# Kernel tuning notes

Hardware: AMD Instinct MI355X
Metric: run time of the kernel (lower is better)

Reference implementation:

```python
import jax, jax.numpy as jnp
import numpy as np

B, T, H, S = 64, 512, 768, 128  # batch, seq_len, hidden_size, num_statements


def setup_inputs() -> dict:
    key = jax.random.key(0)
    ks = jax.random.split(key, 6)
    hidden = jax.random.normal(ks[0], (B, T, H), dtype=jnp.float32)
    # per-token statement ids, sorted (statements appear contiguously in source order)
    statements_ids = jnp.sort(jax.random.randint(ks[1], (B, T), 0, S), axis=-1).astype(jnp.int32)
    scale = 1.0 / np.sqrt(H)
    w1 = jax.random.normal(ks[2], (H, H), dtype=jnp.float32) * scale
    b1 = jnp.zeros((H,), dtype=jnp.float32)
    w2 = jax.random.normal(ks[3], (H, H), dtype=jnp.float32) * scale
    b2 = jnp.zeros((H,), dtype=jnp.float32)
    w3 = jax.random.normal(ks[4], (H, 1), dtype=jnp.float32) * scale
    b3 = jnp.zeros((1,), dtype=jnp.float32)
    return {"hidden": hidden, "statements_ids": statements_ids,
            "w1": w1, "b1": b1, "w2": w2, "b2": b2, "w3": w3, "b3": b3}


def _segment_mean(x, sid):
    # x: [T, H], sid: [T] -> [S, H] mean of tokens per statement id
    sums = jax.ops.segment_sum(x, sid, num_segments=S)            # [S, H]
    cnts = jax.ops.segment_sum(jnp.ones((x.shape[0],), x.dtype), sid, num_segments=S)  # [S]
    return sums / jnp.maximum(cnts, 1.0)[:, None]


def reference(hidden, statements_ids, w1, b1, w2, b2, w3, b3):
    # per-statement mean pooling (scatter-mean), vectorized over batch
    pooled = jax.vmap(_segment_mean)(hidden, statements_ids)      # [B, S, H]
    # CodeCoverageMLP: fc1 -> GELU -> fc2 -> GELU -> fc3 -> sigmoid (dropout = eval identity)
    x = jax.nn.gelu(pooled @ w1 + b1, approximate=False)
    x = jax.nn.gelu(x @ w2 + b2, approximate=False)
    preds = jax.nn.sigmoid(x @ w3 + b3)                           # [B, S, 1]
    return preds[..., 0]                                          # [B, S]
```

## Files before the change

kernel.cpp:

```cpp
#include <hip/hip_runtime.h>
#include <stdint.h>

#define NB 64
#define NT 512
#define NH 768
#define NS 128
#define NM (NB*NS)

typedef _Float16 half8 __attribute__((ext_vector_type(8)));
typedef _Float16 half4 __attribute__((ext_vector_type(4)));
typedef __attribute__((ext_vector_type(4))) float f32x4;

__device__ __forceinline__ float gelu_fast(float x) {
  float ax = fabsf(x) * 0.70710678118654752440f;
  float t  = __builtin_amdgcn_rcpf(1.0f + 0.3275911f * ax);
  float e  = __expf(-ax * ax);
  float poly = t * (0.254829592f + t * (-0.284496736f +
               t * (1.421413741f + t * (-1.453152027f + t * 1.061405429f))));
  float erfv = 1.0f - poly * e;
  float phi  = 0.5f * (1.0f + copysignf(erfv, x));
  return x * phi;
}

__device__ __forceinline__ void gll16(const void* g, void* l) {
  __builtin_amdgcn_global_load_lds(
      (__attribute__((address_space(1))) unsigned int*)g,
      (__attribute__((address_space(3))) unsigned int*)l,
      16, 0, 0);
}

__global__ void prep_w_kernel(const float* __restrict__ w1, const float* __restrict__ w2,
                              _Float16* __restrict__ W) {
  int id = blockIdx.x * 256 + threadIdx.x;
  int n  = id % NH;
  int t  = id / NH;
  int kc = t % 96;
  int w  = t / 96;
  const float* src = w ? w2 : w1;
  int k0 = kc * 8;
  half8 h;
#pragma unroll
  for (int i = 0; i < 8; ++i)
    h[i] = (_Float16)src[(size_t)(k0 + i) * NH + n];
  const size_t off = ((((size_t)w * 48 + (n >> 4)) * 96 + kc) * 16 + (n & 15)) * 8;
  *(half8*)&W[off] = h;
}

__global__ __launch_bounds__(192)
void pool_kernel(const float* __restrict__ hidden, const int* __restrict__ sid,
                 _Float16* __restrict__ Ahi, _Float16* __restrict__ Alo) {
  __shared__ int   s_sid[NT];
  __shared__ short s_e0[NS + 1];
  __shared__ float sAcc[8][NH];
  const int b = blockIdx.y, g = blockIdx.x;
  const int tid = threadIdx.x;

  for (int t = tid; t < NT; t += 192) s_sid[t] = sid[b * NT + t];
  __syncthreads();
  for (int t = tid; t < NT; t += 192) {
    const int cur  = s_sid[t];
    const int prev = t ? s_sid[t - 1] : -1;
    for (int s = prev + 1; s <= cur; ++s) s_e0[s] = (short)t;
    if (t == NT - 1)
      for (int s = cur + 1; s <= NS; ++s) s_e0[s] = (short)NT;
  }
#pragma unroll
  for (int i = 0; i < 8; ++i)
    *(f32x4*)&sAcc[0][(i * 192 + tid) * 4] = (f32x4){0.f, 0.f, 0.f, 0.f};
  __syncthreads();

  const int s0 = g * 8;
  const int t0 = s_e0[s0], t1 = s_e0[s0 + 8];
  const int col = tid * 4;
  const float* hb = hidden + (size_t)b * NT * NH + col;

  if (t1 > t0) {
    constexpr int D = 8;
    f32x4 buf[D];
#pragma unroll
    for (int j = 0; j < D; ++j) {
      int tj = t0 + j; if (tj >= t1) tj = t1 - 1;
      buf[j] = *(const f32x4*)(hb + (size_t)tj * NH);
    }
    f32x4 acc = {0.f, 0.f, 0.f, 0.f};
    int cur = s_sid[t0];
    int t = t0;
    for (; t + D <= t1; t += D) {
#pragma unroll
      for (int j = 0; j < D; ++j) {
        f32x4 v = buf[j];
        int tn = t + j + D; if (tn >= t1) tn = t1 - 1;
        buf[j] = *(const f32x4*)(hb + (size_t)tn * NH);
        const int s = s_sid[t + j];
        if (s != cur) {
          *(f32x4*)&sAcc[cur - s0][col] = acc;
          acc = (f32x4){0.f, 0.f, 0.f, 0.f};
          cur = s;
        }
        acc += v;
      }
    }
#pragma unroll
    for (int j = 0; j < D; ++j) {
      if (t + j < t1) {
        f32x4 v = buf[j];
        const int s = s_sid[t + j];
        if (s != cur) {
          *(f32x4*)&sAcc[cur - s0][col] = acc;
          acc = (f32x4){0.f, 0.f, 0.f, 0.f};
          cur = s;
        }
        acc += v;
      }
    }
    *(f32x4*)&sAcc[cur - s0][col] = acc;
  }
  __syncthreads();

#pragma unroll
  for (int s = 0; s < 8; ++s) {
    const int gs = s0 + s;
    const int cnt = s_e0[gs + 1] - s_e0[gs];
    const float inv = 1.0f / (float)(cnt > 0 ? cnt : 1);
    f32x4 v = *(const f32x4*)&sAcc[s][col];
    half4 h, l;
#pragma unroll
    for (int j = 0; j < 4; ++j) {
      float x = v[j] * inv;
      h[j] = (_Float16)x;
      l[j] = (_Float16)(x - (float)h[j]);
    }
    const size_t off = (size_t)(b * NS + gs) * NH + col;
    *(half4*)&Ahi[off] = h;
    *(half4*)&Alo[off] = l;
  }
}

__global__ __launch_bounds__(512, 4)
void mlp_kernel(const _Float16* __restrict__ Ahi, const _Float16* __restrict__ Alo,
                const _Float16* __restrict__ Wp,
                const float* __restrict__ b1, const float* __restrict__ b2,
                const float* __restrict__ w3, const float* __restrict__ b3,
                float* __restrict__ out) {
  __shared__ _Float16 sA[2][4096];
  __shared__ _Float16 sX[32 * NH];
  float (*sP)[32] = (float(*)[32])&sA[0][0];

  const int tid  = threadIdx.x;
  const int lane = tid & 63;
  const int wv   = tid >> 6;
  const int lr   = lane & 15;
  const int lk4  = lane >> 4;
  const int row0 = blockIdx.x * 32;

  const _Float16* W1 = Wp;
  const _Float16* W2 = Wp + (size_t)NH * NH;

  const int str  = wv * 4 + lk4;
  const int scol = (lr * 8) ^ ((str & 7) << 3);
#define STAGE(kt) {                                                           \
    const size_t src = (size_t)(row0 + str) * NH + (kt) * 128 + scol;         \
    gll16(Ahi + src, &sA[0][wv * 512]);                                       \
    gll16(Alo + src, &sA[1][wv * 512]); }

  f32x4 acc1[2][6] = {};
  STAGE(0);
  __syncthreads();
  for (int kt = 0; kt < 6; ++kt) {
    half8 bw[6], bwn[6];
#pragma unroll
    for (int nf = 0; nf < 6; ++nf)
      bw[nf] = *(const half8*)(W1 + ((size_t)(wv * 6 + nf) * 96 + kt * 16 + lk4) * 128 + lr * 8);
#pragma unroll
    for (int kk = 0; kk < 4; ++kk) {
      if (kk < 3) {
#pragma unroll
        for (int nf = 0; nf < 6; ++nf)
          bwn[nf] = *(const half8*)(W1 + ((size_t)(wv * 6 + nf) * 96 + kt * 16 + (kk + 1) * 4 + lk4) * 128 + lr * 8);
      }
#pragma unroll
      for (int mf = 0; mf < 2; ++mf) {
        const int ar = mf * 16 + lr;
        const int ad = ar * 128 + ((kk * 32 + lk4 * 8) ^ ((ar & 7) << 3));
        half8 ah = *(const half8*)&sA[0][ad];
        half8 al = *(const half8*)&sA[1][ad];
#pragma unroll
        for (int nf = 0; nf < 6; ++nf) {
          acc1[mf][nf] = __builtin_amdgcn_mfma_f32_16x16x32_f16(ah, bw[nf], acc1[mf][nf], 0, 0, 0);
          acc1[mf][nf] = __builtin_amdgcn_mfma_f32_16x16x32_f16(al, bw[nf], acc1[mf][nf], 0, 0, 0);
        }
      }
#pragma unroll
      for (int nf = 0; nf < 6; ++nf) bw[nf] = bwn[nf];
    }
    __syncthreads();
    if (kt < 5) {
      STAGE(kt + 1);
      __syncthreads();
    }
  }

#pragma unroll
  for (int nf = 0; nf < 6; ++nf) {
    const int col = wv * 96 + nf * 16 + lr;
    const float bv = b1[col];
#pragma unroll
    for (int mf = 0; mf < 2; ++mf)
#pragma unroll
      for (int r = 0; r < 4; ++r) {
        const int row = mf * 16 + lk4 * 4 + r;
        sX[row * NH + (col ^ ((row & 7) << 3))] = (_Float16)gelu_fast(acc1[mf][nf][r] + bv);
      }
  }
  __syncthreads();

  f32x4 acc2[2][6] = {};
  half8 bw2[6], bw2n[6];
#pragma unroll
  for (int nf = 0; nf < 6; ++nf)
    bw2[nf] = *(const half8*)(W2 + ((size_t)(wv * 6 + nf) * 96 + lk4) * 128 + lr * 8);
  for (int g = 0; g < 24; ++g) {
    if (g < 23) {
#pragma unroll
      for (int nf = 0; nf < 6; ++nf)
        bw2n[nf] = *(const half8*)(W2 + ((size_t)(wv * 6 + nf) * 96 + (g + 1) * 4 + lk4) * 128 + lr * 8);
    }
    const int koff = g * 32 + lk4 * 8;
#pragma unroll
    for (int mf = 0; mf < 2; ++mf) {
      const int ar = mf * 16 + lr;
      half8 a = *(const half8*)&sX[ar * NH + (koff ^ ((ar & 7) << 3))];
#pragma unroll
      for (int nf = 0; nf < 6; ++nf)
        acc2[mf][nf] = __builtin_amdgcn_mfma_f32_16x16x32_f16(a, bw2[nf], acc2[mf][nf], 0, 0, 0);
    }
#pragma unroll
    for (int nf = 0; nf < 6; ++nf) bw2[nf] = bw2n[nf];
  }

  float p[2][4] = {};
#pragma unroll
  for (int nf = 0; nf < 6; ++nf) {
    const int col = wv * 96 + nf * 16 + lr;
    const float bv = b2[col], wvv = w3[col];
#pragma unroll
    for (int mf = 0; mf < 2; ++mf)
#pragma unroll
      for (int r = 0; r < 4; ++r)
        p[mf][r] += gelu_fast(acc2[mf][nf][r] + bv) * wvv;
  }
#pragma unroll
  for (int mf = 0; mf < 2; ++mf)
#pragma unroll
    for (int r = 0; r < 4; ++r) {
      float v = p[mf][r];
      v += __shfl_xor(v, 1, 16);
      v += __shfl_xor(v, 2, 16);
      v += __shfl_xor(v, 4, 16);
      v += __shfl_xor(v, 8, 16);
      if (lr == 0) sP[wv][mf * 16 + lk4 * 4 + r] = v;
    }
  __syncthreads();
  if (tid < 32) {
    float s = b3[0];
#pragma unroll
    for (int w = 0; w < 8; ++w) s += sP[w][tid];
    out[row0 + tid] = 1.0f / (1.0f + expf(-s));
  }
#undef STAGE
}

extern "C" void kernel_launch(void* const* d_in, const int* in_sizes, int n_in,
                              void* d_out, int out_size, void* d_ws, size_t ws_size,
                              hipStream_t stream) {
  (void)in_sizes; (void)n_in; (void)out_size; (void)ws_size;
  const float* hidden = (const float*)d_in[0];
  const int*   sid    = (const int*)d_in[1];
  const float* w1     = (const float*)d_in[2];
  const float* b1     = (const float*)d_in[3];
  const float* w2     = (const float*)d_in[4];
  const float* b2     = (const float*)d_in[5];
  const float* w3     = (const float*)d_in[6];
  const float* b3     = (const float*)d_in[7];
  float* out = (float*)d_out;

  char* p = (char*)d_ws;
  const size_t actE = (size_t)NM * NH;
  _Float16* Ahi = (_Float16*)p; p += actE * 2;
  _Float16* Alo = (_Float16*)p; p += actE * 2;
  _Float16* W   = (_Float16*)p; p += (size_t)2 * NH * NH * 2;

  prep_w_kernel<<<2 * 96 * NH / 256, 256, 0, stream>>>(w1, w2, W);
  pool_kernel<<<dim3(16, NB), 192, 0, stream>>>(hidden, sid, Ahi, Alo);
  mlp_kernel<<<NM / 32, 512, 0, stream>>>(Ahi, Alo, W, b1, b2, w3, b3, out);
}
```

Baseline: 216.4 us.

## Fuse segment-mean pooling into MLP kernel, keeping pooled activations in LDS

```diff
diff --git a/kernel.cpp b/kernel.cpp
--- a/kernel.cpp
+++ b/kernel.cpp
@@ -20,13 +20,6 @@
   float erfv = 1.0f - poly * e;
   float phi  = 0.5f * (1.0f + copysignf(erfv, x));
   return x * phi;
-}
-
-__device__ __forceinline__ void gll16(const void* g, void* l) {
-  __builtin_amdgcn_global_load_lds(
-      (__attribute__((address_space(1))) unsigned int*)g,
-      (__attribute__((address_space(3))) unsigned int*)l,
-      16, 0, 0);
 }
 
 __global__ void prep_w_kernel(const float* __restrict__ w1, const float* __restrict__ w2,
@@ -46,18 +39,29 @@
   *(half8*)&W[off] = h;
 }
 
-__global__ __launch_bounds__(192)
-void pool_kernel(const float* __restrict__ hidden, const int* __restrict__ sid,
-                 _Float16* __restrict__ Ahi, _Float16* __restrict__ Alo) {
-  __shared__ int   s_sid[NT];
-  __shared__ short s_e0[NS + 1];
-  __shared__ float sAcc[8][NH];
-  const int b = blockIdx.y, g = blockIdx.x;
-  const int tid = threadIdx.x;
-
-  for (int t = tid; t < NT; t += 192) s_sid[t] = sid[b * NT + t];
-  __syncthreads();
-  for (int t = tid; t < NT; t += 192) {
+__global__ __launch_bounds__(512)
+void fused_kernel(const float* __restrict__ hidden, const int* __restrict__ sid,
+                  const _Float16* __restrict__ Wp,
+                  const float* __restrict__ b1, const float* __restrict__ b2,
+                  const float* __restrict__ w3, const float* __restrict__ b3,
+                  float* __restrict__ out) {
+  __shared__ float    sAcc[32 * NH];
+  __shared__ _Float16 sX[32 * NH];
+  __shared__ int      s_sid[NT];
+  __shared__ short    s_e0[NS + 1];
+
+  const int tid  = threadIdx.x;
+  const int lane = tid & 63;
+  const int wv   = tid >> 6;
+  const int lr   = lane & 15;
+  const int lk4  = lane >> 4;
+  const int b  = blockIdx.y;
+  const int s0 = blockIdx.x * 32;
+
+  s_sid[tid] = sid[b * NT + tid];
+  __syncthreads();
+  {
+    const int t = tid;
     const int cur  = s_sid[t];
     const int prev = t ? s_sid[t - 1] : -1;
     for (int s = prev + 1; s <= cur; ++s) s_e0[s] = (short)t;
@@ -65,125 +69,111 @@
       for (int s = cur + 1; s <= NS; ++s) s_e0[s] = (short)NT;
   }
 #pragma unroll
-  for (int i = 0; i < 8; ++i)
-    *(f32x4*)&sAcc[0][(i * 192 + tid) * 4] = (f32x4){0.f, 0.f, 0.f, 0.f};
-  __syncthreads();
-
-  const int s0 = g * 8;
-  const int t0 = s_e0[s0], t1 = s_e0[s0 + 8];
-  const int col = tid * 4;
-  const float* hb = hidden + (size_t)b * NT * NH + col;
-
-  if (t1 > t0) {
-    constexpr int D = 8;
-    f32x4 buf[D];
-#pragma unroll
-    for (int j = 0; j < D; ++j) {
-      int tj = t0 + j; if (tj >= t1) tj = t1 - 1;
-      buf[j] = *(const f32x4*)(hb + (size_t)tj * NH);
-    }
-    f32x4 acc = {0.f, 0.f, 0.f, 0.f};
-    int cur = s_sid[t0];
-    int t = t0;
-    for (; t + D <= t1; t += D) {
+  for (int i = 0; i < 12; ++i)
+    *(f32x4*)&sAcc[(i * 512 + tid) * 4] = (f32x4){0.f, 0.f, 0.f, 0.f};
+  __syncthreads();
+
+  if (tid < 384) {
+    const int tg   = (tid >= 192) ? 1 : 0;
+    const int col  = (tid - tg * 192) * 4;
+    const int sg0  = s0 + tg * 16;
+    const int t0 = s_e0[sg0], t1 = s_e0[sg0 + 16];
+    const float* hb = hidden + (size_t)b * NT * NH + col;
+    if (t1 > t0) {
+      constexpr int D = 8;
+      f32x4 buf[D];
 #pragma unroll
       for (int j = 0; j < D; ++j) {
-        f32x4 v = buf[j];
-        int tn = t + j + D; if (tn >= t1) tn = t1 - 1;
-        buf[j] = *(const f32x4*)(hb + (size_t)tn * NH);
-        const int s = s_sid[t + j];
-        if (s != cur) {
-          *(f32x4*)&sAcc[cur - s0][col] = acc;
-          acc = (f32x4){0.f, 0.f, 0.f, 0.f};
-          cur = s;
+        int tj = t0 + j; if (tj >= t1) tj = t1 - 1;
+        buf[j] = *(const f32x4*)(hb + (size_t)tj * NH);
+      }
+      f32x4 acc = {0.f, 0.f, 0.f, 0.f};
+      int cur = s_sid[t0];
+      int t = t0;
+      for (; t + D <= t1; t += D) {
+#pragma unroll
+        for (int j = 0; j < D; ++j) {
+          f32x4 v = buf[j];
+          int tn = t + j + D; if (tn >= t1) tn = t1 - 1;
+          buf[j] = *(const f32x4*)(hb + (size_t)tn * NH);
+          const int s = s_sid[t + j];
+          if (s != cur) {
+            *(f32x4*)&sAcc[(cur - s0) * NH + col] = acc;
+            acc = (f32x4){0.f, 0.f, 0.f, 0.f};
+            cur = s;
+          }
+          acc += v;
         }
-        acc += v;
-      }
-    }
-#pragma unroll
-    for (int j = 0; j < D; ++j) {
-      if (t + j < t1) {
-        f32x4 v = buf[j];
-        const int s = s_sid[t + j];
-        if (s != cur) {
-          *(f32x4*)&sAcc[cur - s0][col] = acc;
-          acc = (f32x4){0.f, 0.f, 0.f, 0.f};
-          cur = s;
+      }
+#pragma unroll
+      for (int j = 0; j < D; ++j) {
+        if (t + j < t1) {
+          f32x4 v = buf[j];
+          const int s = s_sid[t + j];
+          if (s != cur) {
+            *(f32x4*)&sAcc[(cur - s0) * NH + col] = acc;
+            acc = (f32x4){0.f, 0.f, 0.f, 0.f};
+            cur = s;
+          }
+          acc += v;
         }
-        acc += v;
-      }
-    }
-    *(f32x4*)&sAcc[cur - s0][col] = acc;
-  }
-  __syncthreads();
-
-#pragma unroll
-  for (int s = 0; s < 8; ++s) {
-    const int gs = s0 + s;
-    const int cnt = s_e0[gs + 1] - s_e0[gs];
+      }
+      *(f32x4*)&sAcc[(cur - s0) * NH + col] = acc;
+    }
+  }
+  __syncthreads();
+
+  _Float16* Ah = (_Float16*)sAcc;
+  _Float16* Al = Ah + 32 * NH;
+  {
+    const int r  = tid >> 4;
+    const int c0 = (tid & 15) * 48;
+    f32x4 vv[12];
+#pragma unroll
+    for (int i = 0; i < 12; ++i)
+      vv[i] = *(const f32x4*)&sAcc[r * NH + c0 + i * 4];
+    const int cnt = s_e0[s0 + r + 1] - s_e0[s0 + r];
     const float inv = 1.0f / (float)(cnt > 0 ? cnt : 1);
-    f32x4 v = *(const f32x4*)&sAcc[s][col];
-    half4 h, l;
-#pragma unroll
-    for (int j = 0; j < 4; ++j) {
-      float x = v[j] * inv;
-      h[j] = (_Float16)x;
-      l[j] = (_Float16)(x - (float)h[j]);
-    }
-    const size_t off = (size_t)(b * NS + gs) * NH + col;
-    *(half4*)&Ahi[off] = h;
-    *(half4*)&Alo[off] = l;
-  }
-}
-
-__global__ __launch_bounds__(512, 4)
-void mlp_kernel(const _Float16* __restrict__ Ahi, const _Float16* __restrict__ Alo,
-                const _Float16* __restrict__ Wp,
-                const float* __restrict__ b1, const float* __restrict__ b2,
-                const float* __restrict__ w3, const float* __restrict__ b3,
-                float* __restrict__ out) {
-  __shared__ _Float16 sA[2][4096];
-  __shared__ _Float16 sX[32 * NH];
-  float (*sP)[32] = (float(*)[32])&sA[0][0];
-
-  const int tid  = threadIdx.x;
-  const int lane = tid & 63;
-  const int wv   = tid >> 6;
-  const int lr   = lane & 15;
-  const int lk4  = lane >> 4;
-  const int row0 = blockIdx.x * 32;
+    __syncthreads();
+    const int xr = (r & 7) << 3;
+#pragma unroll
+    for (int i = 0; i < 12; ++i) {
+      half4 h, l;
+#pragma unroll
+      for (int j = 0; j < 4; ++j) {
+        float x = vv[i][j] * inv;
+        h[j] = (_Float16)x;
+        l[j] = (_Float16)(x - (float)h[j]);
+      }
+      const int idx = r * NH + ((c0 + i * 4) ^ xr);
+      *(half4*)&Ah[idx] = h;
+      *(half4*)&Al[idx] = l;
+    }
+  }
+  __syncthreads();
 
   const _Float16* W1 = Wp;
   const _Float16* W2 = Wp + (size_t)NH * NH;
 
-  const int str  = wv * 4 + lk4;
-  const int scol = (lr * 8) ^ ((str & 7) << 3);
-#define STAGE(kt) {                                                           \
-    const size_t src = (size_t)(row0 + str) * NH + (kt) * 128 + scol;         \
-    gll16(Ahi + src, &sA[0][wv * 512]);                                       \
-    gll16(Alo + src, &sA[1][wv * 512]); }
-
   f32x4 acc1[2][6] = {};
-  STAGE(0);
-  __syncthreads();
-  for (int kt = 0; kt < 6; ++kt) {
+  {
     half8 bw[6], bwn[6];
 #pragma unroll
     for (int nf = 0; nf < 6; ++nf)
-      bw[nf] = *(const half8*)(W1 + ((size_t)(wv * 6 + nf) * 96 + kt * 16 + lk4) * 128 + lr * 8);
-#pragma unroll
-    for (int kk = 0; kk < 4; ++kk) {
-      if (kk < 3) {
+      bw[nf] = *(const half8*)(W1 + ((size_t)(wv * 6 + nf) * 96 + lk4) * 128 + lr * 8);
+    for (int g = 0; g < 24; ++g) {
+      if (g < 23) {
 #pragma unroll
         for (int nf = 0; nf < 6; ++nf)
-          bwn[nf] = *(const half8*)(W1 + ((size_t)(wv * 6 + nf) * 96 + kt * 16 + (kk + 1) * 4 + lk4) * 128 + lr * 8);
-      }
+          bwn[nf] = *(const half8*)(W1 + ((size_t)(wv * 6 + nf) * 96 + (g + 1) * 4 + lk4) * 128 + lr * 8);
+      }
+      const int koff = g * 32 + lk4 * 8;
 #pragma unroll
       for (int mf = 0; mf < 2; ++mf) {
         const int ar = mf * 16 + lr;
-        const int ad = ar * 128 + ((kk * 32 + lk4 * 8) ^ ((ar & 7) << 3));
-        half8 ah = *(const half8*)&sA[0][ad];
-        half8 al = *(const half8*)&sA[1][ad];
+        const int ad = ar * NH + (koff ^ ((ar & 7) << 3));
+        half8 ah = *(const half8*)&Ah[ad];
+        half8 al = *(const half8*)&Al[ad];
 #pragma unroll
         for (int nf = 0; nf < 6; ++nf) {
           acc1[mf][nf] = __builtin_amdgcn_mfma_f32_16x16x32_f16(ah, bw[nf], acc1[mf][nf], 0, 0, 0);
@@ -193,11 +183,6 @@
 #pragma unroll
       for (int nf = 0; nf < 6; ++nf) bw[nf] = bwn[nf];
     }
-    __syncthreads();
-    if (kt < 5) {
-      STAGE(kt + 1);
-      __syncthreads();
-    }
   }
 
 #pragma unroll
@@ -215,27 +200,29 @@
   __syncthreads();
 
   f32x4 acc2[2][6] = {};
-  half8 bw2[6], bw2n[6];
-#pragma unroll
-  for (int nf = 0; nf < 6; ++nf)
-    bw2[nf] = *(const half8*)(W2 + ((size_t)(wv * 6 + nf) * 96 + lk4) * 128 + lr * 8);
-  for (int g = 0; g < 24; ++g) {
-    if (g < 23) {
-#pragma unroll
-      for (int nf = 0; nf < 6; ++nf)
-        bw2n[nf] = *(const half8*)(W2 + ((size_t)(wv * 6 + nf) * 96 + (g + 1) * 4 + lk4) * 128 + lr * 8);
-    }
-    const int koff = g * 32 + lk4 * 8;
-#pragma unroll
-    for (int mf = 0; mf < 2; ++mf) {
-      const int ar = mf * 16 + lr;
-      half8 a = *(const half8*)&sX[ar * NH + (koff ^ ((ar & 7) << 3))];
-#pragma unroll
-      for (int nf = 0; nf < 6; ++nf)
-        acc2[mf][nf] = __builtin_amdgcn_mfma_f32_16x16x32_f16(a, bw2[nf], acc2[mf][nf], 0, 0, 0);
-    }
-#pragma unroll
-    for (int nf = 0; nf < 6; ++nf) bw2[nf] = bw2n[nf];
+  {
+    half8 bw[6], bwn[6];
+#pragma unroll
+    for (int nf = 0; nf < 6; ++nf)
+      bw[nf] = *(const half8*)(W2 + ((size_t)(wv * 6 + nf) * 96 + lk4) * 128 + lr * 8);
+    for (int g = 0; g < 24; ++g) {
+      if (g < 23) {
+#pragma unroll
+        for (int nf = 0; nf < 6; ++nf)
+          bwn[nf] = *(const half8*)(W2 + ((size_t)(wv * 6 + nf) * 96 + (g + 1) * 4 + lk4) * 128 + lr * 8);
+      }
+      const int koff = g * 32 + lk4 * 8;
+#pragma unroll
+      for (int mf = 0; mf < 2; ++mf) {
+        const int ar = mf * 16 + lr;
+        half8 a = *(const half8*)&sX[ar * NH + (koff ^ ((ar & 7) << 3))];
+#pragma unroll
+        for (int nf = 0; nf < 6; ++nf)
+          acc2[mf][nf] = __builtin_amdgcn_mfma_f32_16x16x32_f16(a, bw[nf], acc2[mf][nf], 0, 0, 0);
+      }
+#pragma unroll
+      for (int nf = 0; nf < 6; ++nf) bw[nf] = bwn[nf];
+    }
   }
 
   float p[2][4] = {};
@@ -249,6 +236,7 @@
       for (int r = 0; r < 4; ++r)
         p[mf][r] += gelu_fast(acc2[mf][nf][r] + bv) * wvv;
   }
+  float (*sP)[32] = (float(*)[32])s_sid;
 #pragma unroll
   for (int mf = 0; mf < 2; ++mf)
 #pragma unroll
@@ -265,9 +253,8 @@
     float s = b3[0];
 #pragma unroll
     for (int w = 0; w < 8; ++w) s += sP[w][tid];
-    out[row0 + tid] = 1.0f / (1.0f + expf(-s));
-  }
-#undef STAGE
+    out[b * NS + s0 + tid] = 1.0f / (1.0f + expf(-s));
+  }
 }
 
 extern "C" void kernel_launch(void* const* d_in, const int* in_sizes, int n_in,
@@ -284,13 +271,8 @@
   const float* b3     = (const float*)d_in[7];
   float* out = (float*)d_out;
 
-  char* p = (char*)d_ws;
-  const size_t actE = (size_t)NM * NH;
-  _Float16* Ahi = (_Float16*)p; p += actE * 2;
-  _Float16* Alo = (_Float16*)p; p += actE * 2;
-  _Float16* W   = (_Float16*)p; p += (size_t)2 * NH * NH * 2;
+  _Float16* W = (_Float16*)d_ws;
 
   prep_w_kernel<<<2 * 96 * NH / 256, 256, 0, stream>>>(w1, w2, W);
-  pool_kernel<<<dim3(16, NB), 192, 0, stream>>>(hidden, sid, Ahi, Alo);
-  mlp_kernel<<<NM / 32, 512, 0, stream>>>(Ahi, Alo, W, b1, b2, w3, b3, out);
-}
+  fused_kernel<<<dim3(4, NB), 512, 0, stream>>>(hidden, sid, W, b1, b2, w3, b3, out);
+}
```

Result: faster. 203.7 us (-5.9%).
